# Performance work log

Hardware: AMD Instinct MI355X
Metric: run time of the kernel (lower is better)

Reference implementation:

```python
import jax, jax.numpy as jnp
import numpy as np

NUM_HEADS = 12


def _rope(t, cos, sin):
    # t: (B, H, M, D); cos/sin: (M, D//2) applied to interleaved pairs
    B, H, M, D = t.shape
    t2 = t.reshape(B, H, M, D // 2, 2)
    t0, t1 = t2[..., 0], t2[..., 1]
    c = cos[None, None]  # (1,1,M,D//2)
    s = sin[None, None]
    r0 = t0 * c - t1 * s
    r1 = t0 * s + t1 * c
    return jnp.stack([r0, r1], axis=-1).reshape(B, H, M, D)


def setup_inputs() -> dict:
    key = jax.random.key(0)
    ks = jax.random.split(key, 7)
    B, N, C = 16, 577, 768
    Hd = C // NUM_HEADS
    x = jax.random.normal(ks[0], (B, N, C), dtype=jnp.float32)
    # rotary angles for N-1 non-CLS tokens
    theta = jax.random.uniform(ks[1], (N - 1, Hd // 2), dtype=jnp.float32) * 6.28318
    cos = jnp.cos(theta)
    sin = jnp.sin(theta)
    w_qkv = jax.random.normal(ks[2], (C, 3 * C), dtype=jnp.float32) * 0.02
    b_qkv = jax.random.normal(ks[3], (3 * C,), dtype=jnp.float32) * 0.02
    w_proj = jax.random.normal(ks[4], (C, C), dtype=jnp.float32) * 0.02
    b_proj = jax.random.normal(ks[5], (C,), dtype=jnp.float32) * 0.02
    return {"x": x, "cos": cos, "sin": sin, "w_qkv": w_qkv, "b_qkv": b_qkv,
            "w_proj": w_proj, "b_proj": b_proj}


def reference(x, cos, sin, w_qkv, b_qkv, w_proj, b_proj):
    B, N, C = x.shape
    H = NUM_HEADS
    D = C // H
    scale = D ** -0.5
    qkv = x @ w_qkv + b_qkv                       # (B, N, 3C)
    qkv = qkv.reshape(B, N, 3, H, D).transpose(2, 0, 3, 1, 4)  # (3, B, H, N, D)
    q, k, v = qkv[0], qkv[1], qkv[2]
    # RoPE applied to all tokens except the CLS token (index 0)
    q = jnp.concatenate([q[:, :, :1], _rope(q[:, :, 1:], cos, sin)], axis=2)
    k = jnp.concatenate([k[:, :, :1], _rope(k[:, :, 1:], cos, sin)], axis=2)
    attn = jax.nn.softmax(jnp.einsum('bhnd,bhmd->bhnm', q, k) * scale, axis=-1)
    out = jnp.einsum('bhnm,bhmd->bhnd', attn, v)  # (B, H, N, D)
    out = out.transpose(0, 2, 1, 3).reshape(B, N, C)
    return out @ w_proj + b_proj
```

## Files before the change

kernel.cpp:

```cpp
#include <hip/hip_runtime.h>
#include <stdint.h>

typedef unsigned short u16;
typedef __attribute__((ext_vector_type(8))) short bf16x8;
typedef __attribute__((ext_vector_type(4))) float f32x4;

#define MFMA16(a, b, c) __builtin_amdgcn_mfma_f32_16x16x32_bf16((a), (b), (c), 0, 0, 0)

__device__ __forceinline__ float b2f(u16 u) {
    union { unsigned int i; float f; } v; v.i = ((unsigned int)u) << 16; return v.f;
}
__device__ __forceinline__ u16 f2b(float f) {
    union { float f; unsigned int i; } v; v.f = f;
    unsigned int r = v.i + 0x7fffu + ((v.i >> 16) & 1u);
    return (u16)(r >> 16);
}
__device__ __forceinline__ float exp2_fast(float x) {
    float r; __asm__("v_exp_f32 %0, %1" : "=v"(r) : "v"(x)); return r;
}

typedef __attribute__((address_space(1))) void gvoid;
typedef __attribute__((address_space(3))) void lvoid;
__device__ __forceinline__ void gld16(const void* g, void* l) {
    __builtin_amdgcn_global_load_lds((gvoid*)(void*)g, (lvoid*)l, 16, 0, 0);
}

__device__ __forceinline__ void tile_from_bid(int bid, int nTM, int nTN,
                                              int& rt, int& ct) {
    const int PW = 8;
    const int full = nTM / PW;
    const int per = PW * nTN;
    int p = bid / per;
    int pw = PW;
    int rem = bid - p * per;
    if (p >= full) { p = full; rem = bid - full * per; pw = nTM - full * PW; }
    const int c = rem / pw;
    const int r = rem - c * pw;
    rt = p * PW + r;
    ct = c;
}

__global__ __launch_bounds__(256) void f32_to_bf16(const float* __restrict__ in,
                                                   u16* __restrict__ out, int n) {
    const int i = (blockIdx.x * 256 + threadIdx.x) * 4;
    if (i + 3 < n) {
        const float4 v = *(const float4*)(in + i);
        ushort4 o;
        o.x = f2b(v.x); o.y = f2b(v.y); o.z = f2b(v.z); o.w = f2b(v.w);
        *(ushort4*)(out + i) = o;
    }
}

__global__ __launch_bounds__(256) void transpose_w(const float* __restrict__ wqkv,
                                                   const float* __restrict__ wproj,
                                                   u16* __restrict__ outQ,
                                                   u16* __restrict__ outP) {
    __shared__ float tile[32][33];
    int bx = blockIdx.x;
    const float* in; u16* out; int C;
    if (bx < 72) { in = wqkv; out = outQ; C = 2304; }
    else         { bx -= 72; in = wproj; out = outP; C = 768; }
    const int R = 768;
    const int t = threadIdx.x;
    const int r = t >> 3, c4 = (t & 7) * 4;
    const int ir = blockIdx.y * 32 + r, ic = bx * 32 + c4;
    const float4 v = *(const float4*)(in + (size_t)ir * C + ic);
    tile[r][c4 + 0] = v.x; tile[r][c4 + 1] = v.y;
    tile[r][c4 + 2] = v.z; tile[r][c4 + 3] = v.w;
    __syncthreads();
    const int orow = bx * 32 + r, ocol = blockIdx.y * 32 + c4;
    ushort4 o;
    o.x = f2b(tile[c4 + 0][r]); o.y = f2b(tile[c4 + 1][r]);
    o.z = f2b(tile[c4 + 2][r]); o.w = f2b(tile[c4 + 3][r]);
    *(ushort4*)(out + (size_t)orow * R + ocol) = o;
}

template <int EPI>
__global__ __launch_bounds__(512) void gemm_bt(const u16* __restrict__ A,
                                               const u16* __restrict__ Bt,
                                               const float* __restrict__ bias,
                                               void* __restrict__ Cv,
                                               const float* __restrict__ cosp,
                                               const float* __restrict__ sinp,
                                               u16* __restrict__ VtG,
                                               int M, int N, int K) {
    __shared__ __align__(16) u16 As0[128 * 64];
    __shared__ __align__(16) u16 As1[128 * 64];
    __shared__ __align__(16) u16 Bs0[128 * 64];
    __shared__ __align__(16) u16 Bs1[128 * 64];

    const int t = threadIdx.x;
    const int lane = t & 63;
    const int wave = t >> 6;
    const int l15 = lane & 15, quad = lane >> 4;
    const int wm = wave >> 2;
    const int wn = wave & 3;

    int rt, ct;
    tile_from_bid(blockIdx.y * gridDim.x + blockIdx.x, gridDim.x, gridDim.y, rt, ct);
    const int row0 = rt * 128;
    const int col0 = ct * 128;

    const f32x4 fz = {0.f, 0.f, 0.f, 0.f};
    f32x4 acc[4][2];
#pragma unroll
    for (int i = 0; i < 4; ++i)
#pragma unroll
        for (int j = 0; j < 2; ++j) acc[i][j] = fz;

    const u16* Ap[2];
    const u16* Bp[2];
    int off[2];
#pragma unroll
    for (int n = 0; n < 2; ++n) {
        const int g = t + n * 512;
        const int row = g >> 3;
        const int slot = (g & 7) ^ (row & 7);
        int ar = row0 + row; if (ar > M - 1) ar = M - 1;
        Ap[n] = A + (size_t)ar * K + slot * 8;
        Bp[n] = Bt + (size_t)(col0 + row) * K + slot * 8;
        off[n] = g * 8;
    }

#define STAGE(kt_, Ad, Bd) do {                                            \
        const int kb_ = (kt_) << 6;                                        \
        gld16(Ap[0] + kb_, (Ad) + off[0]);                                 \
        gld16(Ap[1] + kb_, (Ad) + off[1]);                                 \
        gld16(Bp[0] + kb_, (Bd) + off[0]);                                 \
        gld16(Bp[1] + kb_, (Bd) + off[1]);                                 \
    } while (0)

#define COMPUTE(Asb, Bsb) do {                                             \
        _Pragma("unroll")                                                  \
        for (int kk = 0; kk < 2; ++kk) {                                   \
            const int swk = ((kk * 4 + quad) ^ (l15 & 7)) * 8;             \
            bf16x8 af[4], bfr[2];                                          \
            _Pragma("unroll")                                              \
            for (int mi = 0; mi < 4; ++mi)                                 \
                af[mi] = *(const bf16x8*)((Asb) +                          \
                    ((wm * 4 + mi) * 16 + l15) * 64 + swk);                \
            _Pragma("unroll")                                              \
            for (int ni = 0; ni < 2; ++ni)                                 \
                bfr[ni] = *(const bf16x8*)((Bsb) +                         \
                    ((wn * 2 + ni) * 16 + l15) * 64 + swk);                \
            _Pragma("unroll")                                              \
            for (int mi = 0; mi < 4; ++mi)                                 \
                _Pragma("unroll")                                          \
                for (int ni = 0; ni < 2; ++ni)                             \
                    acc[mi][ni] = MFMA16(bfr[ni], af[mi], acc[mi][ni]);    \
        }                                                                  \
    } while (0)

    const int nKT = K >> 6;
    STAGE(0, As0, Bs0);
    __syncthreads();

    for (int kt = 0; kt < nKT; kt += 2) {
        if (kt + 1 < nKT) STAGE(kt + 1, As1, Bs1);
        COMPUTE(As0, Bs0);
        __syncthreads();
        if (kt + 2 < nKT) STAGE(kt + 2, As0, Bs0);
        COMPUTE(As1, Bs1);
        __syncthreads();
    }
#undef STAGE
#undef COMPUTE

    if (EPI == 2) {
        if (col0 >= 1536) {
#pragma unroll
            for (int mi = 0; mi < 4; ++mi) {
                const int row = row0 + wm * 64 + mi * 16 + l15;
                if (row < M) {
                    const int bb = row / 577, n = row - bb * 577;
                    u16* vdst = VtG + (size_t)bb * 491520 + n;
#pragma unroll
                    for (int ni = 0; ni < 2; ++ni) {
                        const int colb = col0 + wn * 32 + ni * 16 + quad * 4;
                        const float4 bv = *(const float4*)(bias + colb);
#pragma unroll
                        for (int r = 0; r < 4; ++r) {
                            const int cv = colb + r - 1536;
                            vdst[(size_t)(cv >> 6) * 40960 + (cv & 63) * 640] =
                                f2b(acc[mi][ni][r] + ((const float*)&bv)[r]);
                        }
                    }
                }
            }
        } else {
#pragma unroll
            for (int mi = 0; mi < 4; ++mi) {
                const int row = row0 + wm * 64 + mi * 16 + l15;
                if (row < M) {
                    const int bb = row / 577, n = row - bb * 577;
                    const bool hr = (n >= 1);
                    const float* cb = cosp + (size_t)(hr ? (n - 1) : 0) * 32;
                    const float* sb = sinp + (size_t)(hr ? (n - 1) : 0) * 32;
                    u16* outp = (u16*)Cv + (size_t)row * 1536;
#pragma unroll
                    for (int ni = 0; ni < 2; ++ni) {
                        const int colb = col0 + wn * 32 + ni * 16 + quad * 4;
                        const float4 bv = *(const float4*)(bias + colb);
                        const int pi = (colb & 63) >> 1;
                        float2 c = *(const float2*)(cb + pi);
                        float2 s = *(const float2*)(sb + pi);
                        if (!hr) { c.x = 1.f; c.y = 1.f; s.x = 0.f; s.y = 0.f; }
                        const float v0 = acc[mi][ni][0] + bv.x;
                        const float v1 = acc[mi][ni][1] + bv.y;
                        const float v2 = acc[mi][ni][2] + bv.z;
                        const float v3 = acc[mi][ni][3] + bv.w;
                        ushort4 o;
                        o.x = f2b(v0 * c.x - v1 * s.x);
                        o.y = f2b(v0 * s.x + v1 * c.x);
                        o.z = f2b(v2 * c.y - v3 * s.y);
                        o.w = f2b(v2 * s.y + v3 * c.y);
                        *(ushort4*)(outp + colb) = o;
                    }
                }
            }
        }
    } else {
#pragma unroll
        for (int ni = 0; ni < 2; ++ni) {
            const int colb = col0 + wn * 32 + ni * 16 + quad * 4;
            const float4 bv = *(const float4*)(bias + colb);
#pragma unroll
            for (int mi = 0; mi < 4; ++mi) {
                const int row = row0 + wm * 64 + mi * 16 + l15;
                if (row < M) {
                    float4 o;
                    o.x = acc[mi][ni][0] + bv.x; o.y = acc[mi][ni][1] + bv.y;
                    o.z = acc[mi][ni][2] + bv.z; o.w = acc[mi][ni][3] + bv.w;
                    *(float4*)((float*)Cv + (size_t)row * N + colb) = o;
                }
            }
        }
    }
}

#define PSTR 72
#define CEXP 0.18033688011112042f

__global__ __launch_bounds__(256) void attn2(const u16* __restrict__ qkv,
                                             const u16* __restrict__ VtG,
                                             u16* __restrict__ aout) {
    __shared__ __align__(16) u16 Ks0[64 * 64];
    __shared__ __align__(16) u16 Ks1[64 * 64];
    __shared__ __align__(16) u16 Vs0[64 * 64];
    __shared__ __align__(16) u16 Vs1[64 * 64];
    __shared__ __align__(16) u16 Pb[4 * 16 * PSTR];

    const int t = threadIdx.x;
    const int lane = t & 63, wave = t >> 6;
    const int l15 = lane & 15, quad = lane >> 4;

    const int bid = blockIdx.x;
    const int swz = (bid & 7) * 240 + (bid >> 3);
    const int bh = swz / 10, qt = swz - bh * 10;
    const int b = bh / 12, h = bh - b * 12;
    const u16* baseQ = qkv + (size_t)b * 577 * 1536 + h * 64;
    const u16* baseK = baseQ + 768;
    const u16* vbase = VtG + (size_t)bh * 64 * 640;

    const int mq = qt * 64 + wave * 16 + l15;
    const int nq = mq < 577 ? mq : 576;
    bf16x8 aq[2];
    aq[0] = *(const bf16x8*)(baseQ + (size_t)nq * 1536 + quad * 8);
    aq[1] = *(const bf16x8*)(baseQ + (size_t)nq * 1536 + 32 + quad * 8);

    const int g0 = t, g1 = t + 256;
    const int r0 = g0 >> 3, r1 = g1 >> 3;
    const int s0 = (g0 & 7) ^ (r0 & 7), s1 = (g1 & 7) ^ (r1 & 7);
    const int o0 = g0 * 8, o1 = g1 * 8;
    const u16* Kp0 = baseK + (size_t)r0 * 1536 + s0 * 8;
    const u16* Kp1 = baseK + (size_t)r1 * 1536 + s1 * 8;
    const u16* Vp0 = vbase + (size_t)r0 * 640 + s0 * 8;
    const u16* Vp1 = vbase + (size_t)r1 * 640 + s1 * 8;
    const u16* K9p0 = baseK + (size_t)576 * 1536 + s0 * 8;
    const u16* K9p1 = baseK + (size_t)576 * 1536 + s1 * 8;

    const int swk0 = (quad ^ (l15 & 7)) * 8;
    const int swk1 = ((4 + quad) ^ (l15 & 7)) * 8;

    u16* Pw = Pb + wave * 16 * PSTR;

    f32x4 oacc[4];
    const f32x4 fz = {0.f, 0.f, 0.f, 0.f};
#pragma unroll
    for (int i = 0; i < 4; ++i) oacc[i] = fz;
    float m1 = -1e30f;
    float l1 = 0.f;

#define ASTAGE(kt_, Kd, Vd) do {                                            \
        gld16(Kp0 + (size_t)(kt_) * 98304, (Kd) + o0);                      \
        gld16(Kp1 + (size_t)(kt_) * 98304, (Kd) + o1);                      \
        gld16(Vp0 + (kt_) * 64, (Vd) + o0);                                 \
        gld16(Vp1 + (kt_) * 64, (Vd) + o1);                                 \
    } while (0)

#define ASTAGE9(Kd, Vd) do {                                                \
        gld16(K9p0, (Kd) + o0);                                             \
        gld16(K9p1, (Kd) + o1);                                             \
        gld16(Vp0 + 576, (Vd) + o0);                                        \
        gld16(Vp1 + 576, (Vd) + o1);                                        \
    } while (0)

#define ATT_TILE(kt_, Kb, Vb, MASKED) do {                                  \
        f32x4 sacc[4];                                                      \
        _Pragma("unroll")                                                   \
        for (int nt = 0; nt < 4; ++nt) {                                    \
            sacc[nt] = fz;                                                  \
            const bf16x8 bk0 = *(const bf16x8*)((Kb) + (nt * 16 + l15) * 64 + swk0); \
            sacc[nt] = MFMA16(bk0, aq[0], sacc[nt]);                        \
            const bf16x8 bk1 = *(const bf16x8*)((Kb) + (nt * 16 + l15) * 64 + swk1); \
            sacc[nt] = MFMA16(bk1, aq[1], sacc[nt]);                        \
        }                                                                   \
        if (MASKED) {                                                       \
            _Pragma("unroll")                                               \
            for (int nt = 0; nt < 4; ++nt)                                  \
                _Pragma("unroll")                                           \
                for (int r = 0; r < 4; ++r)                                 \
                    if (nt * 16 + quad * 4 + r > 0) sacc[nt][r] = -1e30f;   \
        }                                                                   \
        float mA = fmaxf(fmaxf(sacc[0][0], sacc[0][1]), fmaxf(sacc[0][2], sacc[0][3])); \
        float mB = fmaxf(fmaxf(sacc[1][0], sacc[1][1]), fmaxf(sacc[1][2], sacc[1][3])); \
        float mC = fmaxf(fmaxf(sacc[2][0], sacc[2][1]), fmaxf(sacc[2][2], sacc[2][3])); \
        float mD = fmaxf(fmaxf(sacc[3][0], sacc[3][1]), fmaxf(sacc[3][2], sacc[3][3])); \
        float mt = fmaxf(fmaxf(mA, mB), fmaxf(mC, mD));                     \
        mt = fmaxf(mt, __shfl_xor(mt, 16));                                 \
        mt = fmaxf(mt, __shfl_xor(mt, 32));                                 \
        const float mnew = fmaxf(m1, mt);                                   \
        const float alpha = exp2_fast((m1 - mnew) * CEXP);                  \
        m1 = mnew;                                                          \
        const float nmc = -mnew * CEXP;                                     \
        float lsum = 0.f;                                                   \
        _Pragma("unroll")                                                   \
        for (int nt = 0; nt < 4; ++nt) {                                    \
            const float p0 = exp2_fast(__builtin_fmaf(sacc[nt][0], CEXP, nmc)); \
            const float p1 = exp2_fast(__builtin_fmaf(sacc[nt][1], CEXP, nmc)); \
            const float p2 = exp2_fast(__builtin_fmaf(sacc[nt][2], CEXP, nmc)); \
            const float p3 = exp2_fast(__builtin_fmaf(sacc[nt][3], CEXP, nmc)); \
            lsum += (p0 + p1) + (p2 + p3);                                  \
            ushort4 pk;                                                     \
            pk.x = f2b(p0); pk.y = f2b(p1); pk.z = f2b(p2); pk.w = f2b(p3); \
            *(ushort4*)(Pw + l15 * PSTR + nt * 16 + quad * 4) = pk;         \
        }                                                                   \
        _Pragma("unroll")                                                   \
        for (int dt = 0; dt < 4; ++dt) {                                    \
            oacc[dt][0] *= alpha; oacc[dt][1] *= alpha;                     \
            oacc[dt][2] *= alpha; oacc[dt][3] *= alpha;                     \
        }                                                                   \
        __asm__ __volatile__("s_waitcnt lgkmcnt(0)" ::: "memory");          \
        _Pragma("unroll")                                                   \
        for (int kc = 0; kc < 2; ++kc) {                                    \
            const bf16x8 pf = *(const bf16x8*)(Pw + l15 * PSTR + kc * 32 + quad * 8); \
            const int swkv = kc ? swk1 : swk0;                              \
            _Pragma("unroll")                                               \
            for (int dt = 0; dt < 4; ++dt) {                                \
                const bf16x8 vf = *(const bf16x8*)((Vb) + (dt * 16 + l15) * 64 + swkv); \
                oacc[dt] = MFMA16(vf, pf, oacc[dt]);                        \
            }                                                               \
        }                                                                   \
        lsum += __shfl_xor(lsum, 16);                                       \
        lsum += __shfl_xor(lsum, 32);                                       \
        l1 = l1 * alpha + lsum;                                             \
    } while (0)

    ASTAGE(0, Ks0, Vs0);
    __syncthreads();

    for (int kt2 = 0; kt2 < 8; kt2 += 2) {
        ASTAGE(kt2 + 1, Ks1, Vs1);
        ATT_TILE(kt2, Ks0, Vs0, false);
        __syncthreads();
        ASTAGE(kt2 + 2, Ks0, Vs0);
        ATT_TILE(kt2 + 1, Ks1, Vs1, false);
        __syncthreads();
    }
    ASTAGE9(Ks1, Vs1);
    ATT_TILE(8, Ks0, Vs0, false);
    __syncthreads();
    ATT_TILE(9, Ks1, Vs1, true);

#undef ASTAGE
#undef ASTAGE9
#undef ATT_TILE

    const int n = qt * 64 + wave * 16 + l15;
    if (n < 577) {
        const float linv = 1.f / l1;
        u16* op = aout + ((size_t)b * 577 + n) * 768 + h * 64 + quad * 4;
#pragma unroll
        for (int dt = 0; dt < 4; ++dt) {
            ushort4 o;
            o.x = f2b(oacc[dt][0] * linv); o.y = f2b(oacc[dt][1] * linv);
            o.z = f2b(oacc[dt][2] * linv); o.w = f2b(oacc[dt][3] * linv);
            *(ushort4*)(op + dt * 16) = o;
        }
    }
}

extern "C" void kernel_launch(void* const* d_in, const int* in_sizes, int n_in,
                              void* d_out, int out_size, void* d_ws, size_t ws_size,
                              hipStream_t stream) {
    const float* x      = (const float*)d_in[0];
    const float* cosp   = (const float*)d_in[1];
    const float* sinp   = (const float*)d_in[2];
    const float* w_qkv  = (const float*)d_in[3];
    const float* b_qkv  = (const float*)d_in[4];
    const float* w_proj = (const float*)d_in[5];
    const float* b_proj = (const float*)d_in[6];
    float* out = (float*)d_out;

    char* ws = (char*)d_ws;
    u16* xb     = (u16*)(ws);
    u16* aout   = (u16*)(ws);
    u16* wqkvT  = (u16*)(ws + 14180352);
    u16* wprojT = (u16*)(ws + 17719296);
    u16* qkv    = (u16*)(ws + 18898944);
    u16* VtG    = (u16*)(ws + 47259648);

    f32_to_bf16<<<6924, 256, 0, stream>>>(x, xb, 7090176);
    transpose_w<<<dim3(96, 24), 256, 0, stream>>>(w_qkv, w_proj, wqkvT, wprojT);
    gemm_bt<2><<<dim3(73, 18), 512, 0, stream>>>(xb, wqkvT, b_qkv, qkv,
                                                 cosp, sinp, VtG, 9232, 2304, 768);
    attn2<<<dim3(1920), 256, 0, stream>>>(qkv, VtG, aout);
    gemm_bt<1><<<dim3(73, 6), 512, 0, stream>>>(aout, wprojT, b_proj, out,
                                                nullptr, nullptr, nullptr, 9232, 768, 768);
}
```

Measured before the change: 218.0 us.

## Enlarge GEMM tiles to 256x128 with triple-buffered LDS pipeline

The GEMM block tile grows from 128x128 to 256x128, so each wave computes a 64x64 sub-tile (4x4 MFMA accumulators) and reuses more data per LDS fragment load. The double-buffered loop becomes a fully unrolled triple-buffered pipeline with a compile-time K-tile count, explicit vmcnt waits and a single barrier per step. Grid swizzle width and launch grids are adjusted to match. The aim is less LDS and global traffic per FLOP and fewer barriers; the costs are 144KB of LDS limiting occupancy, more accumulator registers, and fewer blocks (37x6 for the projection GEMM), which may underfill the CUs.

```diff
diff --git a/kernel.cpp b/kernel.cpp
--- a/kernel.cpp
+++ b/kernel.cpp
@@ -27,7 +27,7 @@
 
 __device__ __forceinline__ void tile_from_bid(int bid, int nTM, int nTN,
                                               int& rt, int& ct) {
-    const int PW = 8;
+    const int PW = 4;
     const int full = nTM / PW;
     const int per = PW * nTN;
     int p = bid / per;
@@ -75,7 +75,7 @@
     *(ushort4*)(out + (size_t)orow * R + ocol) = o;
 }
 
-template <int EPI>
+template <int EPI, int NKT>
 __global__ __launch_bounds__(512) void gemm_bt(const u16* __restrict__ A,
                                                const u16* __restrict__ Bt,
                                                const float* __restrict__ bias,
@@ -84,87 +84,95 @@
                                                const float* __restrict__ sinp,
                                                u16* __restrict__ VtG,
                                                int M, int N, int K) {
-    __shared__ __align__(16) u16 As0[128 * 64];
-    __shared__ __align__(16) u16 As1[128 * 64];
-    __shared__ __align__(16) u16 Bs0[128 * 64];
-    __shared__ __align__(16) u16 Bs1[128 * 64];
+    __shared__ __align__(16) u16 As[3][256 * 64];
+    __shared__ __align__(16) u16 Bs[3][128 * 64];
 
     const int t = threadIdx.x;
     const int lane = t & 63;
     const int wave = t >> 6;
     const int l15 = lane & 15, quad = lane >> 4;
-    const int wm = wave >> 2;
-    const int wn = wave & 3;
+    const int wm = wave >> 1;
+    const int wn = wave & 1;
 
     int rt, ct;
     tile_from_bid(blockIdx.y * gridDim.x + blockIdx.x, gridDim.x, gridDim.y, rt, ct);
-    const int row0 = rt * 128;
+    const int row0 = rt * 256;
     const int col0 = ct * 128;
 
     const f32x4 fz = {0.f, 0.f, 0.f, 0.f};
-    f32x4 acc[4][2];
+    f32x4 acc[4][4];
 #pragma unroll
     for (int i = 0; i < 4; ++i)
 #pragma unroll
-        for (int j = 0; j < 2; ++j) acc[i][j] = fz;
-
-    const u16* Ap[2];
-    const u16* Bp[2];
-    int off[2];
-#pragma unroll
-    for (int n = 0; n < 2; ++n) {
+        for (int j = 0; j < 4; ++j) acc[i][j] = fz;
+
+    const u16* Ap[4]; int offA[4];
+    const u16* Bp[2]; int offB[2];
+#pragma unroll
+    for (int n = 0; n < 4; ++n) {
         const int g = t + n * 512;
         const int row = g >> 3;
         const int slot = (g & 7) ^ (row & 7);
         int ar = row0 + row; if (ar > M - 1) ar = M - 1;
         Ap[n] = A + (size_t)ar * K + slot * 8;
+        offA[n] = g * 8;
+    }
+#pragma unroll
+    for (int n = 0; n < 2; ++n) {
+        const int g = t + n * 512;
+        const int row = g >> 3;
+        const int slot = (g & 7) ^ (row & 7);
         Bp[n] = Bt + (size_t)(col0 + row) * K + slot * 8;
-        off[n] = g * 8;
-    }
-
-#define STAGE(kt_, Ad, Bd) do {                                            \
+        offB[n] = g * 8;
+    }
+
+#define STG(kt_, b_) do {                                                  \
         const int kb_ = (kt_) << 6;                                        \
-        gld16(Ap[0] + kb_, (Ad) + off[0]);                                 \
-        gld16(Ap[1] + kb_, (Ad) + off[1]);                                 \
-        gld16(Bp[0] + kb_, (Bd) + off[0]);                                 \
-        gld16(Bp[1] + kb_, (Bd) + off[1]);                                 \
+        gld16(Ap[0] + kb_, As[b_] + offA[0]);                              \
+        gld16(Ap[1] + kb_, As[b_] + offA[1]);                              \
+        gld16(Ap[2] + kb_, As[b_] + offA[2]);                              \
+        gld16(Ap[3] + kb_, As[b_] + offA[3]);                              \
+        gld16(Bp[0] + kb_, Bs[b_] + offB[0]);                              \
+        gld16(Bp[1] + kb_, Bs[b_] + offB[1]);                              \
     } while (0)
 
-#define COMPUTE(Asb, Bsb) do {                                             \
+#define CMP(b_) do {                                                       \
         _Pragma("unroll")                                                  \
         for (int kk = 0; kk < 2; ++kk) {                                   \
             const int swk = ((kk * 4 + quad) ^ (l15 & 7)) * 8;             \
-            bf16x8 af[4], bfr[2];                                          \
+            bf16x8 af[4], bfr[4];                                          \
             _Pragma("unroll")                                              \
             for (int mi = 0; mi < 4; ++mi)                                 \
-                af[mi] = *(const bf16x8*)((Asb) +                          \
+                af[mi] = *(const bf16x8*)(As[b_] +                         \
                     ((wm * 4 + mi) * 16 + l15) * 64 + swk);                \
             _Pragma("unroll")                                              \
-            for (int ni = 0; ni < 2; ++ni)                                 \
-                bfr[ni] = *(const bf16x8*)((Bsb) +                         \
-                    ((wn * 2 + ni) * 16 + l15) * 64 + swk);                \
+            for (int ni = 0; ni < 4; ++ni)                                 \
+                bfr[ni] = *(const bf16x8*)(Bs[b_] +                        \
+                    ((wn * 4 + ni) * 16 + l15) * 64 + swk);                \
             _Pragma("unroll")                                              \
             for (int mi = 0; mi < 4; ++mi)                                 \
                 _Pragma("unroll")                                          \
-                for (int ni = 0; ni < 2; ++ni)                             \
+                for (int ni = 0; ni < 4; ++ni)                             \
                     acc[mi][ni] = MFMA16(bfr[ni], af[mi], acc[mi][ni]);    \
         }                                                                  \
     } while (0)
 
-    const int nKT = K >> 6;
-    STAGE(0, As0, Bs0);
-    __syncthreads();
-
-    for (int kt = 0; kt < nKT; kt += 2) {
-        if (kt + 1 < nKT) STAGE(kt + 1, As1, Bs1);
-        COMPUTE(As0, Bs0);
-        __syncthreads();
-        if (kt + 2 < nKT) STAGE(kt + 2, As0, Bs0);
-        COMPUTE(As1, Bs1);
-        __syncthreads();
-    }
-#undef STAGE
-#undef COMPUTE
+    STG(0, 0);
+    STG(1, 1);
+#pragma unroll
+    for (int kt = 0; kt < NKT; ++kt) {
+        if (kt == NKT - 1) {
+            __asm__ __volatile__("s_waitcnt vmcnt(0)" ::: "memory");
+        } else {
+            __asm__ __volatile__("s_waitcnt vmcnt(6)" ::: "memory");
+        }
+        __builtin_amdgcn_sched_barrier(0);
+        __builtin_amdgcn_s_barrier();
+        if (kt + 2 < NKT) STG(kt + 2, (kt + 2) % 3);
+        CMP(kt % 3);
+    }
+#undef STG
+#undef CMP
 
     if (EPI == 2) {
         if (col0 >= 1536) {
@@ -175,8 +183,8 @@
                     const int bb = row / 577, n = row - bb * 577;
                     u16* vdst = VtG + (size_t)bb * 491520 + n;
 #pragma unroll
-                    for (int ni = 0; ni < 2; ++ni) {
-                        const int colb = col0 + wn * 32 + ni * 16 + quad * 4;
+                    for (int ni = 0; ni < 4; ++ni) {
+                        const int colb = col0 + wn * 64 + ni * 16 + quad * 4;
                         const float4 bv = *(const float4*)(bias + colb);
 #pragma unroll
                         for (int r = 0; r < 4; ++r) {
@@ -198,8 +206,8 @@
                     const float* sb = sinp + (size_t)(hr ? (n - 1) : 0) * 32;
                     u16* outp = (u16*)Cv + (size_t)row * 1536;
 #pragma unroll
-                    for (int ni = 0; ni < 2; ++ni) {
-                        const int colb = col0 + wn * 32 + ni * 16 + quad * 4;
+                    for (int ni = 0; ni < 4; ++ni) {
+                        const int colb = col0 + wn * 64 + ni * 16 + quad * 4;
                         const float4 bv = *(const float4*)(bias + colb);
                         const int pi = (colb & 63) >> 1;
                         float2 c = *(const float2*)(cb + pi);
@@ -221,8 +229,8 @@
         }
     } else {
 #pragma unroll
-        for (int ni = 0; ni < 2; ++ni) {
-            const int colb = col0 + wn * 32 + ni * 16 + quad * 4;
+        for (int ni = 0; ni < 4; ++ni) {
+            const int colb = col0 + wn * 64 + ni * 16 + quad * 4;
             const float4 bv = *(const float4*)(bias + colb);
 #pragma unroll
             for (int mi = 0; mi < 4; ++mi) {
@@ -422,9 +430,9 @@
 
     f32_to_bf16<<<6924, 256, 0, stream>>>(x, xb, 7090176);
     transpose_w<<<dim3(96, 24), 256, 0, stream>>>(w_qkv, w_proj, wqkvT, wprojT);
-    gemm_bt<2><<<dim3(73, 18), 512, 0, stream>>>(xb, wqkvT, b_qkv, qkv,
-                                                 cosp, sinp, VtG, 9232, 2304, 768);
+    gemm_bt<2, 12><<<dim3(37, 18), 512, 0, stream>>>(xb, wqkvT, b_qkv, qkv,
+                                                     cosp, sinp, VtG, 9232, 2304, 768);
     attn2<<<dim3(1920), 256, 0, stream>>>(qkv, VtG, aout);
-    gemm_bt<1><<<dim3(73, 6), 512, 0, stream>>>(aout, wprojT, b_proj, out,
-                                                nullptr, nullptr, nullptr, 9232, 768, 768);
-}
+    gemm_bt<1, 12><<<dim3(37, 6), 512, 0, stream>>>(aout, wprojT, b_proj, out,
+                                                    nullptr, nullptr, nullptr, 9232, 768, 768);
+}
```

New measurement: 219.3 us. No clear change (+0.6%).

## Replace double-buffered K/V LDS staging with single buffer in attention kernel

Applied to the files above, without the earlier changes.

The attention kernel drops its ping-pong K/V shared-memory buffers and loads each tile into a single buffer, with a barrier before and after every tile's compute. This halves the K/V LDS footprint, which could let more blocks fit per CU. In exchange, global-to-LDS loads no longer overlap with the MFMA work of the previous tile, and each tile now needs two barriers.

```diff
diff --git a/kernel.cpp b/kernel.cpp
--- a/kernel.cpp
+++ b/kernel.cpp
@@ -244,10 +244,8 @@
 __global__ __launch_bounds__(256) void attn2(const u16* __restrict__ qkv,
                                              const u16* __restrict__ VtG,
                                              u16* __restrict__ aout) {
-    __shared__ __align__(16) u16 Ks0[64 * 64];
-    __shared__ __align__(16) u16 Ks1[64 * 64];
-    __shared__ __align__(16) u16 Vs0[64 * 64];
-    __shared__ __align__(16) u16 Vs1[64 * 64];
+    __shared__ __align__(16) u16 Ks[64 * 64];
+    __shared__ __align__(16) u16 Vs[64 * 64];
     __shared__ __align__(16) u16 Pb[4 * 16 * PSTR];
 
     const int t = threadIdx.x;
@@ -291,28 +289,28 @@
     float m1 = -1e30f;
     float l1 = 0.f;
 
-#define ASTAGE(kt_, Kd, Vd) do {                                            \
-        gld16(Kp0 + (size_t)(kt_) * 98304, (Kd) + o0);                      \
-        gld16(Kp1 + (size_t)(kt_) * 98304, (Kd) + o1);                      \
-        gld16(Vp0 + (kt_) * 64, (Vd) + o0);                                 \
-        gld16(Vp1 + (kt_) * 64, (Vd) + o1);                                 \
+#define ASTAGE(kt_) do {                                                    \
+        gld16(Kp0 + (size_t)(kt_) * 98304, Ks + o0);                        \
+        gld16(Kp1 + (size_t)(kt_) * 98304, Ks + o1);                        \
+        gld16(Vp0 + (kt_) * 64, Vs + o0);                                   \
+        gld16(Vp1 + (kt_) * 64, Vs + o1);                                   \
     } while (0)
 
-#define ASTAGE9(Kd, Vd) do {                                                \
-        gld16(K9p0, (Kd) + o0);                                             \
-        gld16(K9p1, (Kd) + o1);                                             \
-        gld16(Vp0 + 576, (Vd) + o0);                                        \
-        gld16(Vp1 + 576, (Vd) + o1);                                        \
+#define ASTAGE9() do {                                                      \
+        gld16(K9p0, Ks + o0);                                               \
+        gld16(K9p1, Ks + o1);                                               \
+        gld16(Vp0 + 576, Vs + o0);                                          \
+        gld16(Vp1 + 576, Vs + o1);                                          \
     } while (0)
 
-#define ATT_TILE(kt_, Kb, Vb, MASKED) do {                                  \
+#define ATT_TILE(kt_, MASKED) do {                                          \
         f32x4 sacc[4];                                                      \
         _Pragma("unroll")                                                   \
         for (int nt = 0; nt < 4; ++nt) {                                    \
             sacc[nt] = fz;                                                  \
-            const bf16x8 bk0 = *(const bf16x8*)((Kb) + (nt * 16 + l15) * 64 + swk0); \
+            const bf16x8 bk0 = *(const bf16x8*)(Ks + (nt * 16 + l15) * 64 + swk0); \
             sacc[nt] = MFMA16(bk0, aq[0], sacc[nt]);                        \
-            const bf16x8 bk1 = *(const bf16x8*)((Kb) + (nt * 16 + l15) * 64 + swk1); \
+            const bf16x8 bk1 = *(const bf16x8*)(Ks + (nt * 16 + l15) * 64 + swk1); \
             sacc[nt] = MFMA16(bk1, aq[1], sacc[nt]);                        \
         }                                                                   \
         if (MASKED) {                                                       \
@@ -357,7 +355,7 @@
             const int swkv = kc ? swk1 : swk0;                              \
             _Pragma("unroll")                                               \
             for (int dt = 0; dt < 4; ++dt) {                                \
-                const bf16x8 vf = *(const bf16x8*)((Vb) + (dt * 16 + l15) * 64 + swkv); \
+                const bf16x8 vf = *(const bf16x8*)(Vs + (dt * 16 + l15) * 64 + swkv); \
                 oacc[dt] = MFMA16(vf, pf, oacc[dt]);                        \
             }                                                               \
         }                                                                   \
@@ -366,21 +364,15 @@
         l1 = l1 * alpha + lsum;                                             \
     } while (0)
 
-    ASTAGE(0, Ks0, Vs0);
+    for (int kt = 0; kt < 9; ++kt) {
+        ASTAGE(kt);
+        __syncthreads();
+        ATT_TILE(kt, false);
+        __syncthreads();
+    }
+    ASTAGE9();
     __syncthreads();
-
-    for (int kt2 = 0; kt2 < 8; kt2 += 2) {
-        ASTAGE(kt2 + 1, Ks1, Vs1);
-        ATT_TILE(kt2, Ks0, Vs0, false);
-        __syncthreads();
-        ASTAGE(kt2 + 2, Ks0, Vs0);
-        ATT_TILE(kt2 + 1, Ks1, Vs1, false);
-        __syncthreads();
-    }
-    ASTAGE9(Ks1, Vs1);
-    ATT_TILE(8, Ks0, Vs0, false);
-    __syncthreads();
-    ATT_TILE(9, Ks1, Vs1, true);
+    ATT_TILE(9, true);
 
 #undef ASTAGE
 #undef ASTAGE9
```

Result: no change. 221.1 us (+1.4%).
